# Performance work log

Hardware: AMD Instinct MI355X
Metric: run time of the kernel (lower is better)

Reference implementation:

```python
import jax, jax.numpy as jnp
import numpy as np

N_P, N_W, F_IN = 512, 3584, 256
H1, O1 = 8, 32
H2, O2 = 8, 256
BATCH = 1024
NEG_SLOPE = 0.2


def _xavier(key, shape):
    fan_in, fan_out = shape[-2], shape[-1]
    lim = jnp.sqrt(6.0 / (fan_in + fan_out))
    return jax.random.uniform(key, shape, jnp.float32, -lim, lim)


def setup_inputs() -> dict:
    key = jax.random.key(0)
    ks = jax.random.split(key, 16)
    return {
        "input": jax.random.uniform(ks[0], (BATCH, N_W), jnp.float32),
        "pern_feature": jax.random.normal(ks[1], (N_P, F_IN), jnp.float32),
        "word_feature": jax.random.normal(ks[2], (N_W, F_IN), jnp.float32),
        "w1": _xavier(ks[3], (H1, F_IN, O1)),
        "a_src1": _xavier(ks[4], (H1, O1, 1)),
        "a_dst1": _xavier(ks[5], (H1, O1, 1)),
        "b1": jnp.zeros((O1,), jnp.float32),
        "w2": _xavier(ks[6], (H2, F_IN, O2)),
        "a_src2": _xavier(ks[7], (H2, F_IN, 1)),
        "a_dst2": _xavier(ks[8], (H2, F_IN, 1)),
        "b2": jnp.zeros((O2,), jnp.float32),
        "W_fc": _xavier(ks[9], (O2, 5)),
        "b_fc": jnp.zeros((5,), jnp.float32),
        "pern_adj": jax.random.randint(ks[10], (N_P, N_P), 0, 2, jnp.int32),
        "word_pern_adj": jax.random.randint(ks[11], (N_P + N_W, N_P + N_W), 0, 2, jnp.int32),
    }


def gat(h, adj, w, a_src, a_dst, bias):
    # h: [N, f_in], adj: [N, N] int, w: [H, f_in, f_out]
    h_prime = jnp.einsum('nf,hfo->hno', h, w)          # [H, N, O]
    t = jnp.tanh(h_prime)
    s_src = jnp.einsum('hno,hoi->hn', t, a_src)        # [H, N]
    s_dst = jnp.einsum('hno,hoi->hn', t, a_dst)        # [H, N]
    attn = s_src[:, :, None] + s_dst[:, None, :]       # [H, N, N]
    attn = jnp.where(attn >= 0, attn, NEG_SLOPE * attn)  # leaky_relu
    attn = jnp.where(adj[None, :, :] > 0, attn, -jnp.inf)
    attn = jax.nn.softmax(attn, axis=-1)
    out = jnp.einsum('hnm,hmo->hno', attn, h_prime)    # [H, N, O]
    return out + bias


def reference(input, pern_feature, word_feature, w1, a_src1, a_dst1, b1,
              w2, a_src2, a_dst2, b2, W_fc, b_fc, pern_adj, word_pern_adj):
    n_p = pern_feature.shape[0]
    # GAT 1 over personality graph
    h1 = gat(pern_feature, pern_adj, w1, a_src1, a_dst1, b1)       # [H1, n_p, O1]
    hiddn_pp = jnp.transpose(h1, (1, 0, 2)).reshape(n_p, -1)        # [n_p, H1*O1]
    hiddn_pp = jax.nn.elu(hiddn_pp)
    # dropout is identity in eval mode
    hiddn_wp = jnp.concatenate([word_feature, hiddn_pp], axis=0)    # [N, 256]
    h2 = gat(hiddn_wp, word_pern_adj, w2, a_src2, a_dst2, b2)       # [H2, N, O2]
    hiddn_wp2 = h2.mean(axis=0)                                     # [N, O2]
    hiddn_w = hiddn_wp2[:word_feature.shape[0], :]                  # [n_w, O2]
    x = (input @ hiddn_w) / input.sum(axis=1, keepdims=True)        # [B, O2]
    return x @ W_fc + b_fc                                          # [B, 5]
```

## Files before the change

### kernel.cpp

```cpp
#include <hip/hip_runtime.h>
#include <hip/hip_bf16.h>
#include <math.h>

#define NP 512
#define NW 3584
#define NT 4096
#define FIN 256
#define H1 8
#define O1 32
#define H2 8
#define O2 256
#define NEG 0.2f

typedef __attribute__((ext_vector_type(8))) short bf16x8;
typedef __attribute__((ext_vector_type(4))) float f32x4;
typedef unsigned long long u64;

__device__ __forceinline__ unsigned short f2bf(float f) {
    unsigned u = __float_as_uint(f);
    unsigned r = (u + 0x7FFF + ((u >> 16) & 1)) >> 16;
    return (unsigned short)r;
}
__device__ __forceinline__ float rflf(float x) {
    return __uint_as_float(__builtin_amdgcn_readfirstlane(__float_as_uint(x)));
}

__global__ __launch_bounds__(256) void k_prep(
    const float* __restrict__ wf, const float* __restrict__ pf,
    const float* __restrict__ w1, const float* __restrict__ a_src1,
    const float* __restrict__ a_dst1, const float* __restrict__ w2,
    const float* __restrict__ b2, const float* __restrict__ W_fc,
    const float* __restrict__ a_src2, const float* __restrict__ a_dst2,
    const int* __restrict__ wp_adj,
    unsigned short* __restrict__ abf, unsigned short* __restrict__ btbf,
    float* __restrict__ hp1, float* __restrict__ ss1, float* __restrict__ sd1,
    unsigned* __restrict__ maskT, float* __restrict__ cvec,
    float* __restrict__ wtab)
{
    __shared__ float tile[64][65];
    __shared__ float feat[2][FIN];
    __shared__ float red[4][5];
    int blk = blockIdx.x;
    int t = threadIdx.x;
    if (blk < 896) {
        int idx4 = blk * 256 + t;
        float4 x = ((const float4*)wf)[idx4];
        ushort4 y;
        y.x = f2bf(x.x); y.y = f2bf(x.y); y.z = f2bf(x.z); y.w = f2bf(x.w);
        ((ushort4*)abf)[idx4] = y;
    } else if (blk < 1152) {
        int n0 = (blk - 896) * 2;
        feat[0][t] = pf[n0 * FIN + t];
        feat[1][t] = pf[(n0 + 1) * FIN + t];
        __syncthreads();
        int h = t >> 5, o = t & 31;
        float acc0 = 0.f, acc1 = 0.f;
        const float* wcol = w1 + h * FIN * O1 + o;
        #pragma unroll 4
        for (int f = 0; f < FIN; f++) {
            float w = wcol[f * O1];
            acc0 += feat[0][f] * w;
            acc1 += feat[1][f] * w;
        }
        hp1[n0 * 256 + t] = acc0;
        hp1[(n0 + 1) * 256 + t] = acc1;
        float as = a_src1[h * O1 + o];
        float ad = a_dst1[h * O1 + o];
        float accs[2] = {acc0, acc1};
        #pragma unroll
        for (int i = 0; i < 2; i++) {
            float th = tanhf(accs[i]);
            float vs = th * as, vd = th * ad;
            #pragma unroll
            for (int off = 1; off < 32; off <<= 1) {
                vs += __shfl_xor(vs, off);
                vd += __shfl_xor(vd, off);
            }
            if (o == 0) { ss1[h * NP + n0 + i] = vs; sd1[h * NP + n0 + i] = vd; }
        }
    } else if (blk < 1280) {
        int blk2 = blk - 1152;
        int h = blk2 >> 4;
        int f0 = ((blk2 >> 2) & 3) * 64;
        int o0 = (blk2 & 3) * 64;
        #pragma unroll
        for (int rr = 0; rr < 16; rr++) {
            int f = rr * 4 + (t >> 6);
            int o = t & 63;
            tile[f][o] = w2[((size_t)(h * FIN + f0 + f)) * O2 + o0 + o];
        }
        __syncthreads();
        #pragma unroll
        for (int rr = 0; rr < 16; rr++) {
            int o = rr * 4 + (t >> 6);
            int f = t & 63;
            btbf[((size_t)(h * O2 + o0 + o)) * FIN + f0 + f] = f2bf(tile[f][o]);
        }
    } else if (blk < 2176) {
        int w = t >> 6, l = t & 63;
        int r = (blk - 1280) * 4 + w;
        const int4* row = (const int4*)(wp_adj + (size_t)r * NT);
        for (int c4 = 0; c4 < 16; c4++) {
            int4 x = row[c4 * 64 + l];
            u64 nib = (u64)((x.x != 0 ? 1 : 0) | (x.y != 0 ? 2 : 0) |
                            (x.z != 0 ? 4 : 0) | (x.w != 0 ? 8 : 0));
            u64 v = nib << (4 * (l & 15));
            v |= __shfl_xor(v, 1);
            v |= __shfl_xor(v, 2);
            v |= __shfl_xor(v, 4);
            v |= __shfl_xor(v, 8);
            if ((l & 15) == 0) {
                int qw = c4 * 4 + (l >> 4);
                maskT[(size_t)(2 * qw) * NW + r]     = (unsigned)v;
                maskT[(size_t)(2 * qw + 1) * NW + r] = (unsigned)(v >> 32);
            }
        }
    } else if (blk == 2176) {
        float v[5];
        #pragma unroll
        for (int j = 0; j < 5; j++) v[j] = b2[t] * W_fc[t * 5 + j];
        #pragma unroll
        for (int off = 1; off < 64; off <<= 1)
            #pragma unroll
            for (int j = 0; j < 5; j++) v[j] += __shfl_xor(v[j], off);
        int w = t >> 6, l = t & 63;
        if (l == 0) { for (int j = 0; j < 5; j++) red[w][j] = v[j]; }
        __syncthreads();
        if (t == 0)
            for (int j = 0; j < 5; j++) cvec[j] = red[0][j] + red[1][j] + red[2][j] + red[3][j];
    } else {
        int h = blk - 2177;
        int o = t;
        float* dst = wtab + ((size_t)h * O2 + o) * 8;
        float4 d0 = {a_src2[h * O2 + o], a_dst2[h * O2 + o], W_fc[o * 5], W_fc[o * 5 + 1]};
        float4 d1 = {W_fc[o * 5 + 2], W_fc[o * 5 + 3], W_fc[o * 5 + 4], 0.f};
        *(float4*)dst = d0;
        *(float4*)(dst + 4) = d1;
    }
}

__global__ __launch_bounds__(256) void k_gat1_attn(
    const int* __restrict__ adj, const float* __restrict__ hp1,
    const float* __restrict__ ss1, const float* __restrict__ sd1,
    const float* __restrict__ b1, unsigned short* __restrict__ abf)
{
    __shared__ float p[2][H1][NP];
    __shared__ float den[2][H1];
    int t = threadIdx.x;
    int n0 = blockIdx.x * 2;
    for (int rr = 0; rr < 32; rr++) {
        int idx = rr * 256 + t;
        int i = idx >> 12, h = (idx >> 9) & 7, m = idx & 511;
        float a = adj[(n0 + i) * NP + m] > 0 ? 1.0f : 0.0f;
        float e = ss1[h * NP + n0 + i] + sd1[h * NP + m];
        e = fmaxf(e, NEG * e);
        p[i][h][m] = a * __expf(e);
    }
    __syncthreads();
    int w = t >> 6, l = t & 63;
    {
        int i = w & 1;
        #pragma unroll
        for (int hh = 0; hh < 4; hh++) {
            int h = (w >> 1) * 4 + hh;
            float s = 0;
            #pragma unroll
            for (int q = 0; q < 8; q++) s += p[i][h][l + 64 * q];
            #pragma unroll
            for (int off = 1; off < 64; off <<= 1) s += __shfl_xor(s, off);
            if (l == 0) den[i][h] = s;
        }
    }
    __syncthreads();
    int h = t >> 5, o = t & 31;
    float a0a = 0.f, a0b = 0.f, a1a = 0.f, a1b = 0.f;
    #pragma unroll 8
    for (int m = 0; m < NP; m += 2) {
        float v0 = hp1[m * 256 + t];
        float v1 = hp1[(m + 1) * 256 + t];
        a0a += p[0][h][m] * v0;
        a1a += p[1][h][m] * v0;
        a0b += p[0][h][m + 1] * v1;
        a1b += p[1][h][m + 1] * v1;
    }
    float acc[2] = {a0a + a0b, a1a + a1b};
    float bo = b1[o];
    #pragma unroll
    for (int i = 0; i < 2; i++) {
        float r = acc[i] / den[i][h] + bo;
        r = r > 0.f ? r : expm1f(r);
        abf[(NW + n0 + i) * FIN + t] = f2bf(r);
    }
}

__global__ __launch_bounds__(256) void k_gemm_hp2(
    const unsigned short* __restrict__ abf, const unsigned short* __restrict__ btbf,
    const float* __restrict__ wtab, float* __restrict__ gpart)
{
    __shared__ unsigned short As[64][264];
    int b = blockIdx.x;
    int h = b & 7, mt = b >> 3;
    int t = threadIdx.x;
    int w = t >> 6, l = t & 63;
    int m0 = mt * 64;
    {
        int row = t >> 5;
        int col8 = (t & 31) * 8;
        #pragma unroll
        for (int u = 0; u < 8; u++)
            *(bf16x8*)(&As[u * 8 + row][col8]) =
                *(const bf16x8*)(abf + (size_t)(m0 + u * 8 + row) * FIN + col8);
    }
    __syncthreads();
    int n0 = w * 64;
    int lr = l & 15, lq = l >> 4;
    const unsigned short* bbase = btbf + h * O2 * FIN;
    f32x4 acc[4][4];
    #pragma unroll
    for (int i = 0; i < 4; i++)
        #pragma unroll
        for (int j = 0; j < 4; j++) acc[i][j] = (f32x4){0.f, 0.f, 0.f, 0.f};
    #pragma unroll
    for (int k = 0; k < FIN; k += 32) {
        bf16x8 a[4], bf[4];
        int kc = k + lq * 8;
        #pragma unroll
        for (int j = 0; j < 4; j++)
            bf[j] = *(const bf16x8*)(bbase + (size_t)(n0 + j * 16 + lr) * FIN + kc);
        #pragma unroll
        for (int i = 0; i < 4; i++)
            a[i] = *(const bf16x8*)(&As[i * 16 + lr][kc]);
        #pragma unroll
        for (int i = 0; i < 4; i++)
            #pragma unroll
            for (int j = 0; j < 4; j++)
                acc[i][j] = __builtin_amdgcn_mfma_f32_16x16x32_bf16(bf[j], a[i], acc[i][j], 0, 0, 0);
    }
    const float* wt = wtab + (size_t)h * O2 * 8;
    float* base = gpart + ((size_t)h * 4 + w) * NT * 8;
    #pragma unroll
    for (int i = 0; i < 4; i++) {
        float s[7] = {0,0,0,0,0,0,0};
        #pragma unroll
        for (int j = 0; j < 4; j++) {
            #pragma unroll
            for (int r = 0; r < 4; r++) {
                float x = acc[i][j][r];
                float ex = __expf(2.0f * x);
                float th = 1.0f - 2.0f * __builtin_amdgcn_rcpf(ex + 1.0f);
                const float* wp = wt + (size_t)(n0 + j * 16 + lq * 4 + r) * 8;
                float4 wa = *(const float4*)wp;
                float4 wb = *(const float4*)(wp + 4);
                s[0] += th * wa.x;
                s[1] += th * wa.y;
                s[2] += x * wa.z;
                s[3] += x * wa.w;
                s[4] += x * wb.x;
                s[5] += x * wb.y;
                s[6] += x * wb.z;
            }
        }
        #pragma unroll
        for (int q = 0; q < 7; q++) {
            s[q] += __shfl_xor(s[q], 16);
            s[q] += __shfl_xor(s[q], 32);
        }
        if (lq == 0) {
            int m = m0 + i * 16 + lr;
            float* dst = base + (size_t)m * 8;
            #pragma unroll
            for (int q = 0; q < 7; q++) dst[q] = s[q];
        }
    }
}

__global__ __launch_bounds__(256) void k_comb_hp2(
    const float* __restrict__ gpart,
    float* __restrict__ Etab, float* __restrict__ Eptab, float* __restrict__ T)
{
    int idx = blockIdx.x * 256 + threadIdx.x;
    float s[7] = {0,0,0,0,0,0,0};
    #pragma unroll
    for (int sl = 0; sl < 4; sl++) {
        const float* p = gpart + (((size_t)(idx >> 12) * 4 + sl) * NT + (idx & (NT - 1))) * 8;
        #pragma unroll
        for (int q = 0; q < 7; q++) s[q] += p[q];
    }
    Etab[idx]  = __expf(s[0]);
    Eptab[idx] = __expf(NEG * s[0]);
    float4 t0 = {__expf(s[1]), __expf(NEG * s[1]), 1.0f, s[2]};
    float4 t1 = {s[3], s[4], s[5], s[6]};
    *(float4*)(T + (size_t)idx * 8)     = t0;
    *(float4*)(T + (size_t)idx * 8 + 4) = t1;
}

__global__ __launch_bounds__(256) void k_gat2_attn(
    const unsigned* __restrict__ maskT, const float* __restrict__ Etab,
    const float* __restrict__ Eptab, const float* __restrict__ T,
    float* __restrict__ part)
{
    __shared__ unsigned pw[64 * 32];
    int t = threadIdx.x;
    int w = t >> 6, l = t & 63;
    int b = blockIdx.x;
    int nb = b % 112;
    int h  = (b / 112) & 7;
    int c  = b / 896;
    int rbase = nb * 32;
    #pragma unroll
    for (int u = 0; u < 8; u++) {
        int idx = u * 256 + t;
        int wd = idx >> 5, row = idx & 31;
        pw[idx] = maskT[(size_t)(c * 64 + wd) * NW + rbase + row];
    }
    __syncthreads();
    int n0 = rbase + w * 8;
    float E[8], Ep[8];
    #pragma unroll
    for (int i = 0; i < 8; i++) {
        int r = h * NT + n0 + i;
        E[i]  = rflf(Etab[r]);
        Ep[i] = rflf(Eptab[r]);
    }
    float den[8] = {0,0,0,0,0,0,0,0};
    float num[8][5] = {{0}};
    const float* Th = T + ((size_t)h * NT + c * 2048) * 8;
    int lsh = l & 31;
    int wdh = l >> 5;
    const unsigned* mbase = pw + w * 8;
    for (int q = 0; q < 32; q++) {
        const float* tp = Th + (size_t)(q * 64 + l) * 8;
        f32x4 t0 = *(const f32x4*)tp;
        f32x4 t1 = *(const f32x4*)(tp + 4);
        int wd = q * 2 + wdh;
        uint4 ma = *(const uint4*)(mbase + wd * 32);
        uint4 mb = *(const uint4*)(mbase + wd * 32 + 4);
        unsigned wv[8] = {ma.x, ma.y, ma.z, ma.w, mb.x, mb.y, mb.z, mb.w};
        #pragma unroll
        for (int i = 0; i < 8; i++) {
            float bm = (float)((wv[i] >> lsh) & 1u);
            float pa = t0.x * E[i];
            float pb = t0.y * Ep[i];
            float pp = fmaxf(pa, pb) * bm;
            den[i] += pp;
            num[i][0] = fmaf(pp, t0.w, num[i][0]);
            num[i][1] = fmaf(pp, t1.x, num[i][1]);
            num[i][2] = fmaf(pp, t1.y, num[i][2]);
            num[i][3] = fmaf(pp, t1.z, num[i][3]);
            num[i][4] = fmaf(pp, t1.w, num[i][4]);
        }
    }
    #pragma unroll
    for (int i = 0; i < 8; i++) {
        float v[6];
        v[0] = den[i];
        #pragma unroll
        for (int j = 0; j < 5; j++) v[1 + j] = num[i][j];
        #pragma unroll
        for (int off = 1; off < 8; off <<= 1)
            #pragma unroll
            for (int k = 0; k < 6; k++) v[k] += __shfl_xor(v[k], off);
        if ((l & 7) == 0) {
            float* dst = part + ((((size_t)c * NW + n0 + i) * 8 + h) * 8 + (l >> 3)) * 8;
            #pragma unroll
            for (int k = 0; k < 6; k++) dst[k] = v[k];
        }
    }
}

__global__ __launch_bounds__(256) void k_gat2_comb(const float* __restrict__ part,
                                                   float* __restrict__ hf) {
    int idx = blockIdx.x * 256 + threadIdx.x;
    int n = idx >> 3, h = idx & 7;
    float den = 0, num[5] = {0,0,0,0,0};
    #pragma unroll
    for (int cc = 0; cc < 2; cc++) {
        #pragma unroll
        for (int s = 0; s < 8; s++) {
            const float* p = part + ((((size_t)cc * NW + n) * 8 + h) * 8 + s) * 8;
            float4 a = *(const float4*)p;
            float4 bq = *(const float4*)(p + 4);
            den += a.x;
            num[0] += a.y; num[1] += a.z; num[2] += a.w;
            num[3] += bq.x; num[4] += bq.y;
        }
    }
    float inv = 1.0f / (den * 8.0f);
    float v[5];
    #pragma unroll
    for (int j = 0; j < 5; j++) v[j] = num[j] * inv;
    #pragma unroll
    for (int off = 1; off < 8; off <<= 1)
        #pragma unroll
        for (int j = 0; j < 5; j++) v[j] += __shfl_xor(v[j], off);
    if (h == 0) {
        #pragma unroll
        for (int j = 0; j < 5; j++) hf[n * 5 + j] = v[j];
    }
}

__global__ __launch_bounds__(256) void k_final(
    const float* __restrict__ input, const float* __restrict__ hf,
    const float* __restrict__ cvec, const float* __restrict__ b_fc,
    float* __restrict__ out)
{
    int b = blockIdx.x, t = threadIdx.x;
    const float4* row4 = (const float4*)(input + (size_t)b * NW);
    const float4* hf4 = (const float4*)hf;
    float s = 0.f, a[5] = {0.f, 0.f, 0.f, 0.f, 0.f};
    for (int idx = t; idx < NW / 4; idx += 256) {
        float4 x = row4[idx];
        float f[20];
        #pragma unroll
        for (int q = 0; q < 5; q++) *(float4*)(f + 4 * q) = hf4[idx * 5 + q];
        s += x.x + x.y + x.z + x.w;
        #pragma unroll
        for (int j = 0; j < 5; j++)
            a[j] += x.x * f[j] + x.y * f[5 + j] + x.z * f[10 + j] + x.w * f[15 + j];
    }
    #pragma unroll
    for (int off = 1; off < 64; off <<= 1) {
        s += __shfl_xor(s, off);
        #pragma unroll
        for (int j = 0; j < 5; j++) a[j] += __shfl_xor(a[j], off);
    }
    __shared__ float red[4][6];
    int w = t >> 6, l = t & 63;
    if (l == 0) { red[w][0] = s; for (int j = 0; j < 5; j++) red[w][j + 1] = a[j]; }
    __syncthreads();
    if (t < 5) {
        float st = red[0][0] + red[1][0] + red[2][0] + red[3][0];
        float aj = red[0][t + 1] + red[1][t + 1] + red[2][t + 1] + red[3][t + 1];
        out[b * 5 + t] = aj / st + cvec[t] + b_fc[t];
    }
}

extern "C" void kernel_launch(void* const* d_in, const int* in_sizes, int n_in,
                              void* d_out, int out_size, void* d_ws, size_t ws_size,
                              hipStream_t stream) {
    const float* input   = (const float*)d_in[0];
    const float* pf      = (const float*)d_in[1];
    const float* wf      = (const float*)d_in[2];
    const float* w1      = (const float*)d_in[3];
    const float* a_src1  = (const float*)d_in[4];
    const float* a_dst1  = (const float*)d_in[5];
    const float* b1      = (const float*)d_in[6];
    const float* w2      = (const float*)d_in[7];
    const float* a_src2  = (const float*)d_in[8];
    const float* a_dst2  = (const float*)d_in[9];
    const float* b2      = (const float*)d_in[10];
    const float* W_fc    = (const float*)d_in[11];
    const float* b_fc    = (const float*)d_in[12];
    const int* pern_adj  = (const int*)d_in[13];
    const int* wp_adj    = (const int*)d_in[14];
    float* out = (float*)d_out;

    char* ws = (char*)d_ws;
    unsigned short* abf    = (unsigned short*)(ws);
    unsigned short* btbf   = (unsigned short*)(ws + 2097152);
    float*          hp1    = (float*)(ws + 3145728);
    float*          ss1    = (float*)(ws + 3670016);
    float*          sd1    = (float*)(ws + 3686400);
    float*          Etab   = (float*)(ws + 3833856);
    float*          Eptab  = (float*)(ws + 3964928);
    float*          T      = (float*)(ws + 4096000);
    float*          hf     = (float*)(ws + 5144576);
    float*          cvec   = (float*)(ws + 5216256);
    unsigned*       maskT  = (unsigned*)(ws + 5216512);
    float*          gpart  = (float*)(ws + 7051520);
    float*          part   = (float*)(ws + 11245824);
    float*          wtab   = (float*)(ws + 26214400);

    k_prep<<<2185, 256, 0, stream>>>(wf, pf, w1, a_src1, a_dst1, w2, b2, W_fc,
                                     a_src2, a_dst2, wp_adj,
                                     abf, btbf, hp1, ss1, sd1, maskT, cvec, wtab);
    k_gat1_attn<<<256, 256, 0, stream>>>(pern_adj, hp1, ss1, sd1, b1, abf);
    k_gemm_hp2<<<512, 256, 0, stream>>>(abf, btbf, wtab, gpart);
    k_comb_hp2<<<128, 256, 0, stream>>>(gpart, Etab, Eptab, T);
    k_gat2_attn<<<1792, 256, 0, stream>>>(maskT, Etab, Eptab, T, part);
    k_gat2_comb<<<112, 256, 0, stream>>>(part, hf);
    k_final<<<1024, 256, 0, stream>>>(input, hf, cvec, b_fc, out);
}
```

Measured before the change: 248.3 us.

## Split GAT attention kernels across more blocks with partial-sum combine passes

GAT1 attention previously ran 256 blocks that each handled two rows over all 512 neighbours. It now runs 1024 blocks, each handling one row and half the neighbours, and a new combine kernel adds the two halves before applying bias, ELU and bf16 conversion. GAT2 attention doubles its column chunks from 2 to 4, giving 3584 blocks with half the inner loop each, and reduces across 32 lanes instead of 8 so fewer partials are written. The aim is higher occupancy and better load balance on the many-CU GPU, at the cost of an extra kernel launch and extra partial-sum traffic.

```diff
diff --git a/kernel.cpp b/kernel.cpp
--- a/kernel.cpp
+++ b/kernel.cpp
@@ -142,55 +142,60 @@
 __global__ __launch_bounds__(256) void k_gat1_attn(
     const int* __restrict__ adj, const float* __restrict__ hp1,
     const float* __restrict__ ss1, const float* __restrict__ sd1,
+    float* __restrict__ g1acc, float* __restrict__ g1den)
+{
+    __shared__ float af[256];
+    __shared__ float p[8][256];
+    __shared__ float den8[8];
+    int t = threadIdx.x;
+    int b = blockIdx.x;
+    int n = b >> 1, mh = b & 1;
+    int mbase = mh * 256;
+    af[t] = adj[n * NP + mbase + t] > 0 ? 1.0f : 0.0f;
+    __syncthreads();
+    #pragma unroll
+    for (int r = 0; r < 8; r++) {
+        int idx = r * 256 + t;
+        int h = idx >> 8, m = idx & 255;
+        float e = ss1[h * NP + n] + sd1[h * NP + mbase + m];
+        e = fmaxf(e, NEG * e);
+        p[h][m] = af[m] * __expf(e);
+    }
+    __syncthreads();
+    int w = t >> 6, l = t & 63;
+    #pragma unroll
+    for (int hh = 0; hh < 2; hh++) {
+        int h = w + hh * 4;
+        float s = 0;
+        #pragma unroll
+        for (int k = 0; k < 4; k++) s += p[h][l + 64 * k];
+        #pragma unroll
+        for (int off = 1; off < 64; off <<= 1) s += __shfl_xor(s, off);
+        if (l == 0) den8[h] = s;
+    }
+    __syncthreads();
+    int h = t >> 5;
+    float acc0 = 0.f, acc1 = 0.f;
+    #pragma unroll 8
+    for (int m = 0; m < 256; m += 2) {
+        acc0 += p[h][m]     * hp1[(mbase + m) * 256 + t];
+        acc1 += p[h][m + 1] * hp1[(mbase + m + 1) * 256 + t];
+    }
+    g1acc[((size_t)mh * NP + n) * 256 + t] = acc0 + acc1;
+    if (t < 8) g1den[((size_t)mh * NP + n) * 8 + t] = den8[t];
+}
+
+__global__ __launch_bounds__(256) void k_gat1_comb(
+    const float* __restrict__ g1acc, const float* __restrict__ g1den,
     const float* __restrict__ b1, unsigned short* __restrict__ abf)
 {
-    __shared__ float p[2][H1][NP];
-    __shared__ float den[2][H1];
-    int t = threadIdx.x;
-    int n0 = blockIdx.x * 2;
-    for (int rr = 0; rr < 32; rr++) {
-        int idx = rr * 256 + t;
-        int i = idx >> 12, h = (idx >> 9) & 7, m = idx & 511;
-        float a = adj[(n0 + i) * NP + m] > 0 ? 1.0f : 0.0f;
-        float e = ss1[h * NP + n0 + i] + sd1[h * NP + m];
-        e = fmaxf(e, NEG * e);
-        p[i][h][m] = a * __expf(e);
-    }
-    __syncthreads();
-    int w = t >> 6, l = t & 63;
-    {
-        int i = w & 1;
-        #pragma unroll
-        for (int hh = 0; hh < 4; hh++) {
-            int h = (w >> 1) * 4 + hh;
-            float s = 0;
-            #pragma unroll
-            for (int q = 0; q < 8; q++) s += p[i][h][l + 64 * q];
-            #pragma unroll
-            for (int off = 1; off < 64; off <<= 1) s += __shfl_xor(s, off);
-            if (l == 0) den[i][h] = s;
-        }
-    }
-    __syncthreads();
+    int n = blockIdx.x, t = threadIdx.x;
     int h = t >> 5, o = t & 31;
-    float a0a = 0.f, a0b = 0.f, a1a = 0.f, a1b = 0.f;
-    #pragma unroll 8
-    for (int m = 0; m < NP; m += 2) {
-        float v0 = hp1[m * 256 + t];
-        float v1 = hp1[(m + 1) * 256 + t];
-        a0a += p[0][h][m] * v0;
-        a1a += p[1][h][m] * v0;
-        a0b += p[0][h][m + 1] * v1;
-        a1b += p[1][h][m + 1] * v1;
-    }
-    float acc[2] = {a0a + a0b, a1a + a1b};
-    float bo = b1[o];
-    #pragma unroll
-    for (int i = 0; i < 2; i++) {
-        float r = acc[i] / den[i][h] + bo;
-        r = r > 0.f ? r : expm1f(r);
-        abf[(NW + n0 + i) * FIN + t] = f2bf(r);
-    }
+    float acc = g1acc[(size_t)n * 256 + t] + g1acc[((size_t)NP + n) * 256 + t];
+    float den = g1den[(size_t)n * 8 + h] + g1den[((size_t)NP + n) * 8 + h];
+    float r = acc / den + b1[o];
+    r = r > 0.f ? r : expm1f(r);
+    abf[(size_t)(NW + n) * FIN + t] = f2bf(r);
 }
 
 __global__ __launch_bounds__(256) void k_gemm_hp2(
@@ -299,7 +304,7 @@
     const float* __restrict__ Eptab, const float* __restrict__ T,
     float* __restrict__ part)
 {
-    __shared__ unsigned pw[64 * 32];
+    __shared__ unsigned pw[32 * 32];
     int t = threadIdx.x;
     int w = t >> 6, l = t & 63;
     int b = blockIdx.x;
@@ -308,10 +313,10 @@
     int c  = b / 896;
     int rbase = nb * 32;
     #pragma unroll
-    for (int u = 0; u < 8; u++) {
+    for (int u = 0; u < 4; u++) {
         int idx = u * 256 + t;
         int wd = idx >> 5, row = idx & 31;
-        pw[idx] = maskT[(size_t)(c * 64 + wd) * NW + rbase + row];
+        pw[idx] = maskT[(size_t)(c * 32 + wd) * NW + rbase + row];
     }
     __syncthreads();
     int n0 = rbase + w * 8;
@@ -324,11 +329,12 @@
     }
     float den[8] = {0,0,0,0,0,0,0,0};
     float num[8][5] = {{0}};
-    const float* Th = T + ((size_t)h * NT + c * 2048) * 8;
+    const float* Th = T + ((size_t)h * NT + c * 1024) * 8;
     int lsh = l & 31;
     int wdh = l >> 5;
     const unsigned* mbase = pw + w * 8;
-    for (int q = 0; q < 32; q++) {
+    #pragma unroll 2
+    for (int q = 0; q < 16; q++) {
         const float* tp = Th + (size_t)(q * 64 + l) * 8;
         f32x4 t0 = *(const f32x4*)tp;
         f32x4 t1 = *(const f32x4*)(tp + 4);
@@ -357,11 +363,11 @@
         #pragma unroll
         for (int j = 0; j < 5; j++) v[1 + j] = num[i][j];
         #pragma unroll
-        for (int off = 1; off < 8; off <<= 1)
+        for (int off = 1; off < 32; off <<= 1)
             #pragma unroll
             for (int k = 0; k < 6; k++) v[k] += __shfl_xor(v[k], off);
-        if ((l & 7) == 0) {
-            float* dst = part + ((((size_t)c * NW + n0 + i) * 8 + h) * 8 + (l >> 3)) * 8;
+        if ((l & 31) == 0) {
+            float* dst = part + ((((size_t)c * NW + n0 + i) * 8 + h) * 2 + (l >> 5)) * 8;
             #pragma unroll
             for (int k = 0; k < 6; k++) dst[k] = v[k];
         }
@@ -374,10 +380,10 @@
     int n = idx >> 3, h = idx & 7;
     float den = 0, num[5] = {0,0,0,0,0};
     #pragma unroll
-    for (int cc = 0; cc < 2; cc++) {
-        #pragma unroll
-        for (int s = 0; s < 8; s++) {
-            const float* p = part + ((((size_t)cc * NW + n) * 8 + h) * 8 + s) * 8;
+    for (int cc = 0; cc < 4; cc++) {
+        #pragma unroll
+        for (int s = 0; s < 2; s++) {
+            const float* p = part + ((((size_t)cc * NW + n) * 8 + h) * 2 + s) * 8;
             float4 a = *(const float4*)p;
             float4 bq = *(const float4*)(p + 4);
             den += a.x;
@@ -468,16 +474,19 @@
     float*          cvec   = (float*)(ws + 5216256);
     unsigned*       maskT  = (unsigned*)(ws + 5216512);
     float*          gpart  = (float*)(ws + 7051520);
-    float*          part   = (float*)(ws + 11245824);
+    float*          g1acc  = (float*)(ws + 11245824);
+    float*          g1den  = (float*)(ws + 12294400);
+    float*          part   = (float*)(ws + 12582912);
     float*          wtab   = (float*)(ws + 26214400);
 
     k_prep<<<2185, 256, 0, stream>>>(wf, pf, w1, a_src1, a_dst1, w2, b2, W_fc,
                                      a_src2, a_dst2, wp_adj,
                                      abf, btbf, hp1, ss1, sd1, maskT, cvec, wtab);
-    k_gat1_attn<<<256, 256, 0, stream>>>(pern_adj, hp1, ss1, sd1, b1, abf);
+    k_gat1_attn<<<1024, 256, 0, stream>>>(pern_adj, hp1, ss1, sd1, g1acc, g1den);
+    k_gat1_comb<<<512, 256, 0, stream>>>(g1acc, g1den, b1, abf);
     k_gemm_hp2<<<512, 256, 0, stream>>>(abf, btbf, wtab, gpart);
     k_comb_hp2<<<128, 256, 0, stream>>>(gpart, Etab, Eptab, T);
-    k_gat2_attn<<<1792, 256, 0, stream>>>(maskT, Etab, Eptab, T, part);
+    k_gat2_attn<<<3584, 256, 0, stream>>>(maskT, Etab, Eptab, T, part);
     k_gat2_comb<<<112, 256, 0, stream>>>(part, hf);
     k_final<<<1024, 256, 0, stream>>>(input, hf, cvec, b_fc, out);
 }
```

Measured after the change: 250.8 us. About the same (+1.0%).
